# Kernel optimization log

Hardware: AMD Instinct MI355X
Metric: run time of the kernel (lower is better)

Reference implementation:

```python
import jax, jax.numpy as jnp
import numpy as np
from jax import lax

HUMAN_CONF = 0.7
IOU_TH = 0.5


def setup_inputs() -> dict:
    key = jax.random.key(0)
    k1, k2 = jax.random.split(key)
    B, Q, C = 16, 2048, 2
    return {
        "human_logits": jax.random.normal(k1, (B, Q, C), dtype=jnp.float32),
        "pred_boxes": jax.random.uniform(k2, (B, Q, 4), dtype=jnp.float32),  # cxcywh in [0,1]
        "img_h": 800,
        "img_w": 1333,
    }


def box_cxcywh_to_xyxy(b):
    cx, cy, w, h = b[..., 0], b[..., 1], b[..., 2], b[..., 3]
    return jnp.stack([cx - 0.5 * w, cy - 0.5 * h, cx + 0.5 * w, cy + 0.5 * h], axis=-1)


def pairwise_iou(b):
    # b: [Q,4] xyxy -> iou: [Q,Q]
    area = jnp.clip(b[:, 2] - b[:, 0], 0) * jnp.clip(b[:, 3] - b[:, 1], 0)
    lt = jnp.maximum(b[:, None, :2], b[None, :, :2])
    rb = jnp.minimum(b[:, None, 2:], b[None, :, 2:])
    wh = jnp.clip(rb - lt, 0)
    inter = wh[..., 0] * wh[..., 1]
    union = area[:, None] + area[None, :] - inter
    return inter / jnp.maximum(union, 1e-9)


def nms_keep(boxes, scores, valid, iou_th):
    # Greedy NMS on one image with fixed shapes; returns keep mask [Q].
    Q = scores.shape[0]
    order = jnp.argsort(jnp.where(valid, -scores, jnp.inf))  # valid boxes first, score desc
    b = boxes[order]
    v = valid[order]
    iou = pairwise_iou(b)                       # [Q,Q]
    idx = jnp.arange(Q)
    sup_mat = (iou > iou_th) & (idx[None, :] > idx[:, None])  # i suppresses later j

    def step(supp, i):
        keep_i = v[i] & jnp.logical_not(supp[i])
        supp = supp | (keep_i & sup_mat[i])
        return supp, keep_i

    _, keep_sorted = lax.scan(step, jnp.zeros(Q, bool), idx)
    return jnp.zeros(Q, bool).at[order].set(keep_sorted)


def reference(human_logits, pred_boxes, img_h, img_w):
    prob = jax.nn.softmax(human_logits, axis=-1)          # [B,Q,C]
    scores = prob.max(axis=-1)                            # [B,Q]
    labels = prob.argmax(axis=-1)                         # [B,Q]
    boxes = box_cxcywh_to_xyxy(pred_boxes)                # [B,Q,4]
    scale = jnp.array([img_w, img_h, img_w, img_h], dtype=boxes.dtype)
    boxes = boxes * scale
    valid = (labels == 0) & (scores >= HUMAN_CONF)
    keep = jax.vmap(lambda b, s, v: nms_keep(b, s, v, IOU_TH))(boxes, scores, valid)
    scores_out = jnp.where(keep, scores, 0.0)
    boxes_out = jnp.where(keep[..., None], boxes, 0.0).astype(jnp.int32)
    return scores_out, boxes_out, keep
```

## Files before the change

### kernel.cpp

```cpp
#include <hip/hip_runtime.h>
#include <math.h>


#define QN    2048
#define NS    1024
#define MATW  17408
#define MAGIC 0x5ca1ab1eu

__device__ __forceinline__ int rb32(int wb) { return 64 * wb * (33 - wb); }

__device__ __forceinline__ unsigned long long shfl_xor_u64(unsigned long long x, int m) {
    int lo = __shfl_xor((int)(unsigned)(x & 0xffffffffull), m, 64);
    int hi = __shfl_xor((int)(unsigned)(x >> 32), m, 64);
    return ((unsigned long long)(unsigned)hi << 32) | (unsigned)lo;
}

__device__ __forceinline__ unsigned long long score_key(float2 l, int q, bool* valid_out) {
    float mx = fmaxf(l.x, l.y), mn = fminf(l.x, l.y);
    float e = expf(mn - mx);
    float score = 1.0f / (1.0f + e);
    bool valid = (l.x >= l.y) && (score >= 0.7f);
    *valid_out = valid;
    unsigned sbits = valid ? __float_as_uint(score) : 0u;
    return ((unsigned long long)(~sbits) << 32) | (unsigned)q;
}

__global__ __launch_bounds__(1024) void kfused(
    const float* __restrict__ logits, const float* __restrict__ pboxes,
    const int* __restrict__ img_h_p, const int* __restrict__ img_w_p,
    unsigned* __restrict__ wflag, unsigned* __restrict__ wmat,
    float* __restrict__ out, int B)
{
    __shared__ __align__(16) char smem[32904];
    unsigned long long* skey = (unsigned long long*)smem;
    float* sx1 = (float*)(smem + 8192);
    float* sy1 = (float*)(smem + 12288);
    float* sx2 = (float*)(smem + 16384);
    float* sy2 = (float*)(smem + 20480);
    float* sar = (float*)(smem + 24576);
    unsigned short* sidxl = (unsigned short*)(smem + 28672);
    unsigned char* keepq = (unsigned char*)(smem + 30720);
    unsigned* skm = (unsigned*)(smem + 32768);
    int* sMp = (int*)(smem + 32896);

    const int blk = blockIdx.x;
    const int b = blk % B, slice = blk / B;
    const int tid = threadIdx.x, lane = tid & 63, wave = tid >> 6;
    const float sw = (float)(*img_w_p), sh = (float)(*img_h_p);

    if (tid == 0) *sMp = 0;
    keepq[tid] = 0; keepq[tid + 1024] = 0;
    if (tid < 32) skm[tid] = 0;
    __syncthreads();

    const unsigned long long lmask_lt = (1ull << lane) - 1ull;
#pragma unroll
    for (int qq = 0; qq < 2; ++qq) {
        int q = tid + qq * 1024;
        float2 l = ((const float2*)logits)[b * QN + q];
        bool valid;
        unsigned long long key = score_key(l, q, &valid);
        unsigned long long mb = __ballot(valid);
        int base = 0;
        if (lane == 0 && mb) base = atomicAdd(sMp, __popcll(mb));
        base = __shfl(base, 0, 64);
        if (valid) {
            int slot = base + __popcll(mb & lmask_lt);
            if (slot < NS) skey[slot] = key;
        }
    }
    __syncthreads();
    const int M = *sMp;

    if (M <= NS) {
        unsigned long long v = (tid < M) ? skey[tid] : ~0ull;
        __syncthreads();
#pragma unroll
        for (int k = 2; k <= 64; k <<= 1) {
            bool dir = ((tid & k) == 0);
#pragma unroll
            for (int j = k >> 1; j > 0; j >>= 1) {
                unsigned long long o = shfl_xor_u64(v, j);
                bool takeMin = (dir == ((tid & j) == 0));
                v = ((v < o) == takeMin) ? v : o;
            }
        }
        for (int k = 128; k <= NS; k <<= 1) {
            bool dir = ((tid & k) == 0);
            for (int j = k >> 1; j >= 64; j >>= 1) {
                skey[tid] = v;
                __syncthreads();
                unsigned long long o = skey[tid ^ j];
                bool takeMin = (dir == ((tid & j) == 0));
                v = ((v < o) == takeMin) ? v : o;
                __syncthreads();
            }
#pragma unroll
            for (int j = 32; j > 0; j >>= 1) {
                unsigned long long o = shfl_xor_u64(v, j);
                bool takeMin = (dir == ((tid & j) == 0));
                v = ((v < o) == takeMin) ? v : o;
            }
        }
        int qi = (int)((unsigned)v & 0xffffu);
        sidxl[tid] = (unsigned short)qi;
        float x1 = 0.f, y1 = 0.f, x2 = 0.f, y2 = 0.f, ar = 0.f;
        if (tid < M) {
            float4 pb = ((const float4*)pboxes)[b * QN + qi];
            x1 = (pb.x - 0.5f * pb.z) * sw;
            y1 = (pb.y - 0.5f * pb.w) * sh;
            x2 = (pb.x + 0.5f * pb.z) * sw;
            y2 = (pb.y + 0.5f * pb.w) * sh;
            ar = fmaxf(x2 - x1, 0.f) * fmaxf(y2 - y1, 0.f);
        }
        sx1[tid] = x1; sy1[tid] = y1; sx2[tid] = x2; sy2[tid] = y2; sar[tid] = ar;
        __syncthreads();

        unsigned* mat = wmat + (long)b * MATW;
        const int NG = (M + 3) >> 2;
        const int W64 = (M + 63) >> 6;
        for (int gi = slice * 16 + wave; gi < NG; gi += 128) {
            const int g = gi << 2;
            const int nr = min(4, M - g);
            const int wb = g >> 6;
            const int rl = 32 - 2 * wb;
            float ax1[4], ay1[4], ax2[4], ay2[4], aar[4];
            int rbase[4];
#pragma unroll
            for (int r = 0; r < 4; ++r) {
                int i = g + min(r, nr - 1);
                ax1[r] = sx1[i]; ay1[r] = sy1[i];
                ax2[r] = sx2[i]; ay2[r] = sy2[i]; aar[r] = sar[i];
                rbase[r] = rb32(wb) + ((g + r) & 63) * rl;
            }
            for (int w = wb; w < W64; ++w) {
                int j = (w << 6) | lane;
                float bx1 = sx1[j], by1 = sy1[j], bx2 = sx2[j], by2 = sy2[j], bar = sar[j];
#pragma unroll
                for (int r = 0; r < 4; ++r) {
                    float ltx = fmaxf(ax1[r], bx1), lty = fmaxf(ay1[r], by1);
                    float rbx = fminf(ax2[r], bx2), rby = fminf(ay2[r], by2);
                    float wx = fmaxf(rbx - ltx, 0.f), wy = fmaxf(rby - lty, 0.f);
                    float inter = wx * wy;
                    float uni = aar[r] + bar - inter;
                    float iou = inter / fmaxf(uni, 1e-9f);
                    bool sup = (iou > 0.5f) && (j > g + r);
                    unsigned long long bal = __ballot(sup);
                    if (lane == 0 && r < nr)
                        *(unsigned long long*)(mat + rbase[r] + 2 * (w - wb)) = bal;
                }
            }
        }
        __syncthreads();
        if (tid == 0)
            __hip_atomic_store(&wflag[b * 8 + slice], MAGIC,
                               __ATOMIC_RELEASE, __HIP_MEMORY_SCOPE_AGENT);
        if (slice != 0) return;

        if (wave == 0) {
            const unsigned* fp = &wflag[b * 8 + (lane & 7)];
            for (;;) {
                unsigned f = (lane < 8)
                    ? __hip_atomic_load(fp, __ATOMIC_ACQUIRE, __HIP_MEMORY_SCOPE_AGENT)
                    : MAGIC;
                if (__all(f == MAGIC)) break;
                __builtin_amdgcn_s_sleep(2);
            }
            const unsigned* gm = wmat + (long)b * MATW;
            unsigned rem = 0;
            const int Ms = __builtin_amdgcn_readfirstlane(M);
            const int C = (Ms + 31) >> 5;
            unsigned rcur[32], rnxt[32];
            if (C > 0) {
                int Lc = min(tid, 31);
#pragma unroll
                for (int t = 0; t < 32; ++t) rcur[t] = gm[Lc + t * 32];
            }
            for (int c = 0; c < C; ++c) {
                if (c + 1 < C) {
                    int cn = c + 1, wbn = cn >> 1, rln = 32 - 2 * wbn;
                    int Lcn = min(max(tid, 2 * wbn), 31);
                    int rb0n = rb32(wbn) + ((cn & 1) << 5) * rln + (Lcn - 2 * wbn);
#pragma unroll
                    for (int t = 0; t < 32; ++t) rnxt[t] = gm[rb0n + t * rln];
                }
                unsigned rw = (unsigned)__builtin_amdgcn_readlane((int)rem, c);
                unsigned keepmask = 0;
                int lim = min(32, Ms - (c << 5));
#pragma unroll
                for (int t = 0; t < 32; ++t) {
                    if (t < lim && !((rw >> t) & 1u)) {
                        keepmask |= (1u << t);
                        rem |= rcur[t];
                        rw |= (unsigned)__builtin_amdgcn_readlane((int)rcur[t], c);
                    }
                }
                if (tid == 0) skm[c] = keepmask;
                if (c + 1 < C) {
#pragma unroll
                    for (int t = 0; t < 32; ++t) rcur[t] = rnxt[t];
                }
            }
        }
        __syncthreads();
        for (int s = tid; s < M; s += 1024)
            if ((skm[s >> 5] >> (s & 31)) & 1u) keepq[sidxl[s]] = 1;
        __syncthreads();
    } else {
        if (slice != 0) return;
        unsigned long long* skeyF = (unsigned long long*)smem;
        unsigned char* ssupp = (unsigned char*)(smem + 16384);
        for (int q = tid; q < QN; q += 1024) {
            float2 l = ((const float2*)logits)[b * QN + q];
            bool valid;
            skeyF[q] = score_key(l, q, &valid);
        }
        __syncthreads();
        for (int k = 2; k <= QN; k <<= 1)
            for (int j = k >> 1; j > 0; j >>= 1) {
                int i = ((tid & ~(j - 1)) << 1) | (tid & (j - 1));
                int p = i | j;
                bool up = ((i & k) == 0);
                unsigned long long a = skeyF[i], c2 = skeyF[p];
                if ((a > c2) == up) { skeyF[i] = c2; skeyF[p] = a; }
                __syncthreads();
            }
        for (int s = tid; s < M; s += 1024) ssupp[s] = 0;
        __syncthreads();
        for (int i = 0; i < M; ++i) {
            __syncthreads();
            if (ssupp[i]) continue;
            int ia = (unsigned short)(unsigned)skeyF[i];
            float4 pa = ((const float4*)pboxes)[b * QN + ia];
            float ax1 = (pa.x - 0.5f * pa.z) * sw, ay1 = (pa.y - 0.5f * pa.w) * sh;
            float ax2 = (pa.x + 0.5f * pa.z) * sw, ay2 = (pa.y + 0.5f * pa.w) * sh;
            float areaA = fmaxf(ax2 - ax1, 0.f) * fmaxf(ay2 - ay1, 0.f);
            for (int jj = i + 1 + tid; jj < M; jj += 1024) {
                int jb = (unsigned short)(unsigned)skeyF[jj];
                float4 pq = ((const float4*)pboxes)[b * QN + jb];
                float bx1 = (pq.x - 0.5f * pq.z) * sw, by1 = (pq.y - 0.5f * pq.w) * sh;
                float bx2 = (pq.x + 0.5f * pq.z) * sw, by2 = (pq.y + 0.5f * pq.w) * sh;
                float ltx = fmaxf(ax1, bx1), lty = fmaxf(ay1, by1);
                float rbx = fminf(ax2, bx2), rby = fminf(ay2, by2);
                float wx = fmaxf(rbx - ltx, 0.f), wy = fmaxf(rby - lty, 0.f);
                float inter = wx * wy;
                float areaB = fmaxf(bx2 - bx1, 0.f) * fmaxf(by2 - by1, 0.f);
                float uni = areaA + areaB - inter;
                if (inter / fmaxf(uni, 1e-9f) > 0.5f) ssupp[jj] = 1;
            }
        }
        __syncthreads();
        for (int s = tid; s < M; s += 1024)
            if (!ssupp[s]) keepq[(unsigned short)(unsigned)skeyF[s]] = 1;
        __syncthreads();
    }

    const long BQ = (long)B * QN;
#pragma unroll
    for (int qq = 0; qq < 2; ++qq) {
        int q = tid + qq * 1024;
        int base = b * QN + q;
        float2 l = ((const float2*)logits)[base];
        float e = expf(fminf(l.x, l.y) - fmaxf(l.x, l.y));
        float score = 1.0f / (1.0f + e);
        float4 pb = ((const float4*)pboxes)[base];
        float x1 = (pb.x - 0.5f * pb.z) * sw, y1 = (pb.y - 0.5f * pb.w) * sh;
        float x2 = (pb.x + 0.5f * pb.z) * sw, y2 = (pb.y + 0.5f * pb.w) * sh;
        int kp = keepq[q];
        out[base] = kp ? score : 0.f;
        out[BQ * 5 + base] = kp ? 1.f : 0.f;
        float4 ob;
        ob.x = kp ? truncf(x1) : 0.f;
        ob.y = kp ? truncf(y1) : 0.f;
        ob.z = kp ? truncf(x2) : 0.f;
        ob.w = kp ? truncf(y2) : 0.f;
        ((float4*)(out + BQ))[base] = ob;
    }
}

extern "C" void kernel_launch(void* const* d_in, const int* in_sizes, int n_in,
                              void* d_out, int out_size, void* d_ws, size_t ws_size,
                              hipStream_t stream) {
    const float* logits = (const float*)d_in[0];
    const float* pboxes = (const float*)d_in[1];
    const int*   img_h  = (const int*)d_in[2];
    const int*   img_w  = (const int*)d_in[3];
    float* out = (float*)d_out;
    const int B = in_sizes[0] / (QN * 2);

    char* ws = (char*)d_ws;
    unsigned* wflag = (unsigned*)(ws + 0);
    unsigned* wmat  = (unsigned*)(ws + 1024);

    kfused<<<dim3(B * 8), dim3(1024), 0, stream>>>(logits, pboxes, img_h, img_w,
                                                   wflag, wmat, out, B);
}
```

Before: 102.9 us.

## Build suppression matrix in LDS with one block per image, drop cross-block flags

Each image's NMS suppression bitmask matrix now lives in shared memory (about 100 KB) instead of global workspace. The image is handled by a single 1024-thread block rather than eight cooperating blocks. This removes the global-memory writes and reads of the matrix and the release/acquire flag spin-wait between slices. The cost is a grid of only B blocks, 16 here, and each block does all of the IoU work alone, which lowers parallelism on a GPU with many CUs. The large LDS allocation also limits each CU to one such block.

```diff
diff --git a/kernel.cpp b/kernel.cpp
--- a/kernel.cpp
+++ b/kernel.cpp
@@ -2,10 +2,10 @@
 #include <math.h>
 
 
-#define QN    2048
-#define NS    1024
-#define MATW  17408
-#define MAGIC 0x5ca1ab1eu
+#define QN     2048
+#define NS     1024
+#define MATW   17408
+#define MATOFF 33024
 
 __device__ __forceinline__ int rb32(int wb) { return 64 * wb * (33 - wb); }
 
@@ -28,10 +28,9 @@
 __global__ __launch_bounds__(1024) void kfused(
     const float* __restrict__ logits, const float* __restrict__ pboxes,
     const int* __restrict__ img_h_p, const int* __restrict__ img_w_p,
-    unsigned* __restrict__ wflag, unsigned* __restrict__ wmat,
     float* __restrict__ out, int B)
 {
-    __shared__ __align__(16) char smem[32904];
+    __shared__ __align__(16) char smem[MATOFF + MATW * 4];
     unsigned long long* skey = (unsigned long long*)smem;
     float* sx1 = (float*)(smem + 8192);
     float* sy1 = (float*)(smem + 12288);
@@ -42,9 +41,9 @@
     unsigned char* keepq = (unsigned char*)(smem + 30720);
     unsigned* skm = (unsigned*)(smem + 32768);
     int* sMp = (int*)(smem + 32896);
-
-    const int blk = blockIdx.x;
-    const int b = blk % B, slice = blk / B;
+    unsigned* mat = (unsigned*)(smem + MATOFF);
+
+    const int b = blockIdx.x;
     const int tid = threadIdx.x, lane = tid & 63, wave = tid >> 6;
     const float sw = (float)(*img_w_p), sh = (float)(*img_h_p);
 
@@ -116,10 +115,9 @@
         sx1[tid] = x1; sy1[tid] = y1; sx2[tid] = x2; sy2[tid] = y2; sar[tid] = ar;
         __syncthreads();
 
-        unsigned* mat = wmat + (long)b * MATW;
         const int NG = (M + 3) >> 2;
         const int W64 = (M + 63) >> 6;
-        for (int gi = slice * 16 + wave; gi < NG; gi += 128) {
+        for (int gi = wave; gi < NG; gi += 16) {
             const int g = gi << 2;
             const int nr = min(4, M - g);
             const int wb = g >> 6;
@@ -152,21 +150,9 @@
             }
         }
         __syncthreads();
-        if (tid == 0)
-            __hip_atomic_store(&wflag[b * 8 + slice], MAGIC,
-                               __ATOMIC_RELEASE, __HIP_MEMORY_SCOPE_AGENT);
-        if (slice != 0) return;
 
         if (wave == 0) {
-            const unsigned* fp = &wflag[b * 8 + (lane & 7)];
-            for (;;) {
-                unsigned f = (lane < 8)
-                    ? __hip_atomic_load(fp, __ATOMIC_ACQUIRE, __HIP_MEMORY_SCOPE_AGENT)
-                    : MAGIC;
-                if (__all(f == MAGIC)) break;
-                __builtin_amdgcn_s_sleep(2);
-            }
-            const unsigned* gm = wmat + (long)b * MATW;
+            const unsigned* gm = mat;
             unsigned rem = 0;
             const int Ms = __builtin_amdgcn_readfirstlane(M);
             const int C = (Ms + 31) >> 5;
@@ -207,7 +193,6 @@
             if ((skm[s >> 5] >> (s & 31)) & 1u) keepq[sidxl[s]] = 1;
         __syncthreads();
     } else {
-        if (slice != 0) return;
         unsigned long long* skeyF = (unsigned long long*)smem;
         unsigned char* ssupp = (unsigned char*)(smem + 16384);
         for (int q = tid; q < QN; q += 1024) {
@@ -288,10 +273,7 @@
     float* out = (float*)d_out;
     const int B = in_sizes[0] / (QN * 2);
 
-    char* ws = (char*)d_ws;
-    unsigned* wflag = (unsigned*)(ws + 0);
-    unsigned* wmat  = (unsigned*)(ws + 1024);
-
-    kfused<<<dim3(B * 8), dim3(1024), 0, stream>>>(logits, pboxes, img_h, img_w,
-                                                   wflag, wmat, out, B);
-}
+    (void)d_ws; (void)ws_size; (void)out_size; (void)n_in;
+
+    kfused<<<dim3(B), dim3(1024), 0, stream>>>(logits, pboxes, img_h, img_w, out, B);
+}
```

Result: slower. 137.4 us (+33.5%).
